# Optimization experiments

Hardware: AMD Instinct MI355X
Metric: run time of the kernel (lower is better)

## Reference

```python
import jax, jax.numpy as jnp
import numpy as np


def l2_normalize(x, eps=1e-12):
    return x / (jnp.linalg.norm(x, axis=-1, keepdims=True) + eps)


def setup_inputs() -> dict:
    key = jax.random.key(0)
    k1, k2, k3 = jax.random.split(key, 3)
    s, n, dim = 16384, 8192, 512
    img_emb = jax.random.normal(k1, (s, dim), dtype=jnp.float32)
    txt_emb = jax.random.normal(k2, (n, dim), dtype=jnp.float32)
    key_idx = jax.random.randint(k3, (s,), 0, n, dtype=jnp.int32)
    t_prime = jnp.asarray(np.log(10.0), dtype=jnp.float32)  # typical SigLIP init
    b = jnp.asarray(-10.0, dtype=jnp.float32)
    return {"img_emb": img_emb, "txt_emb": txt_emb, "key_idx": key_idx,
            "t_prime": t_prime, "b": b}


def reference(img_emb, txt_emb, key_idx, t_prime, b):
    s, dim = img_emb.shape
    n = txt_emb.shape[0]
    t = jnp.exp(t_prime)
    zimg = l2_normalize(img_emb)   # [s, d]
    ztxt = l2_normalize(txt_emb)   # [n, d]

    # [s, n] similarity logits
    all_pairs_logits = jnp.matmul(zimg, ztxt.T) * t + b
    true_positive_logits = all_pairs_logits[jnp.arange(s), key_idx]       # [s]
    potential_positive_losses = jax.nn.softplus(-true_positive_logits)    # [s]

    # grouped argmin over images sharing the same text key (vectorized segmented argmin)
    seg_min = jax.ops.segment_min(potential_positive_losses, key_idx, num_segments=n)  # [n], +inf if empty
    is_best = potential_positive_losses == seg_min[key_idx]                            # [s]
    cand_idx = jnp.where(is_best, jnp.arange(s), s)
    sel = jax.ops.segment_min(cand_idx, key_idx, num_segments=n)  # first minimal index per key; big if empty
    valid = sel < s                                                # [n]
    selected_img_global_indices = jnp.where(valid, sel, -1)
    zimg_selected = jnp.where(valid[:, None],
                              jnp.take(zimg, jnp.clip(sel, 0, s - 1), axis=0),
                              jnp.zeros((), dtype=zimg.dtype))     # [n, d]

    final_logits = jnp.matmul(zimg_selected, ztxt.T) * t + b       # [n, n]
    final_labels = 2.0 * jnp.eye(n, dtype=final_logits.dtype) - 1.0
    loss_terms = jax.nn.softplus(-(final_labels * final_logits))
    final_loss = jnp.sum(loss_terms) / n
    return final_loss, zimg_selected, ztxt, final_logits, selected_img_global_indices
```

## Files before the change

### kernel.cpp

```cpp
#include <hip/hip_runtime.h>
#include <hip/hip_bf16.h>

typedef short short8 __attribute__((ext_vector_type(8)));
typedef float f32x4 __attribute__((ext_vector_type(4)));

#define S_IMG 16384
#define N_TXT 8192
#define DIM   512

#if __has_builtin(__builtin_amdgcn_exp2f)
#define FAST_EXP2(x) __builtin_amdgcn_exp2f(x)
#else
#define FAST_EXP2(x) exp2f(x)
#endif
#if __has_builtin(__builtin_amdgcn_logf)
#define FAST_LOG2(x) __builtin_amdgcn_logf(x)
#else
#define FAST_LOG2(x) log2f(x)
#endif
#if __has_builtin(__builtin_amdgcn_sched_barrier)
#define SCHED_FENCE() __builtin_amdgcn_sched_barrier(0)
#else
#define SCHED_FENCE()
#endif

__device__ inline float softplus_f(float x) {
  float e = FAST_EXP2(-fabsf(x) * 1.44269504088896f);
  return fmaxf(x, 0.f) + 0.69314718055995f * FAST_LOG2(1.0f + e);
}

#define GLOAD16(g, l)                                                   \
  __builtin_amdgcn_global_load_lds(                                     \
      (const __attribute__((address_space(1))) void*)(g),               \
      (__attribute__((address_space(3))) void*)(l), 16, 0, 0)

__device__ inline unsigned short f2bf(float x) {
  unsigned u = __builtin_bit_cast(unsigned, x);
  unsigned r = (u + 0x7FFFu + ((u >> 16) & 1u)) >> 16;
  return (unsigned short)r;
}

__device__ inline double wave_reduce_add_d(double v) {
#pragma unroll
  for (int m = 32; m; m >>= 1) v += __shfl_xor(v, m, 64);
  return v;
}

__global__ __launch_bounds__(256) void k_norm_txt(const float* __restrict__ txt,
                                                  float* __restrict__ ztxt_f32,
                                                  unsigned short* __restrict__ Bbf) {
  int row  = blockIdx.x * 4 + (threadIdx.x >> 6);
  int lane = threadIdx.x & 63;
  const float* src = txt + (size_t)row * DIM;
  float4 v0 = reinterpret_cast<const float4*>(src)[lane];
  float4 v1 = reinterpret_cast<const float4*>(src)[lane + 64];
  double ss = (double)v0.x * v0.x + (double)v0.y * v0.y + (double)v0.z * v0.z + (double)v0.w * v0.w
            + (double)v1.x * v1.x + (double)v1.y * v1.y + (double)v1.z * v1.z + (double)v1.w * v1.w;
  ss = wave_reduce_add_d(ss);
  float sc = (float)(1.0 / (sqrt(ss) + 1e-12));
  float o[8] = {v0.x * sc, v0.y * sc, v0.z * sc, v0.w * sc,
                v1.x * sc, v1.y * sc, v1.z * sc, v1.w * sc};
  float* dst = ztxt_f32 + (size_t)row * DIM;
#pragma unroll
  for (int j = 0; j < 4; ++j) dst[4 * lane + j] = o[j];
#pragma unroll
  for (int j = 0; j < 4; ++j) dst[256 + 4 * lane + j] = o[4 + j];
  ushort4 p0 = make_ushort4(f2bf(o[0]), f2bf(o[1]), f2bf(o[2]), f2bf(o[3]));
  ushort4 p1 = make_ushort4(f2bf(o[4]), f2bf(o[5]), f2bf(o[6]), f2bf(o[7]));
  reinterpret_cast<ushort4*>(Bbf + (size_t)row * DIM)[lane]       = p0;
  reinterpret_cast<ushort4*>(Bbf + (size_t)row * DIM + 256)[lane] = p1;
}

__global__ __launch_bounds__(256) void k_img_loss(const float* __restrict__ img,
                                                  const float* __restrict__ ztxt_f32,
                                                  const int* __restrict__ key_idx,
                                                  const float* __restrict__ tp,
                                                  const float* __restrict__ bp,
                                                  unsigned long long* __restrict__ seg,
                                                  float* __restrict__ invnorm) {
  int row  = blockIdx.x * 4 + (threadIdx.x >> 6);
  int lane = threadIdx.x & 63;
  const float* src = img + (size_t)row * DIM;
  float4 a0 = reinterpret_cast<const float4*>(src)[lane];
  float4 a1 = reinterpret_cast<const float4*>(src)[lane + 64];
  int key = key_idx[row];
  const float* zt = ztxt_f32 + (size_t)key * DIM;
  float z0[4], z1[4];
#pragma unroll
  for (int j = 0; j < 4; ++j) z0[j] = zt[4 * lane + j];
#pragma unroll
  for (int j = 0; j < 4; ++j) z1[j] = zt[256 + 4 * lane + j];
  double ss = (double)a0.x * a0.x + (double)a0.y * a0.y + (double)a0.z * a0.z + (double)a0.w * a0.w
            + (double)a1.x * a1.x + (double)a1.y * a1.y + (double)a1.z * a1.z + (double)a1.w * a1.w;
  double dp = (double)a0.x * z0[0] + (double)a0.y * z0[1] + (double)a0.z * z0[2] + (double)a0.w * z0[3]
            + (double)a1.x * z1[0] + (double)a1.y * z1[1] + (double)a1.z * z1[2] + (double)a1.w * z1[3];
  ss = wave_reduce_add_d(ss);
  dp = wave_reduce_add_d(dp);
  if (lane == 0) {
    double inv = 1.0 / (sqrt(ss) + 1e-12);
    invnorm[row] = (float)inv;
    float t = expf(tp[0]);
    float logit = (float)(dp * inv) * t + bp[0];
    float loss = log1pf(expf(-logit));
    unsigned long long pk =
        ((unsigned long long)__builtin_bit_cast(unsigned, loss) << 32) | (unsigned)row;
    atomicMin(seg + key, pk);
  }
}

__global__ __launch_bounds__(256) void k_select(const float* __restrict__ img,
                                                const unsigned long long* __restrict__ seg,
                                                const float* __restrict__ invnorm,
                                                float* __restrict__ zsel_f32,
                                                float* __restrict__ idx_out,
                                                unsigned short* __restrict__ Abf) {
  int k    = blockIdx.x * 4 + (threadIdx.x >> 6);
  int lane = threadIdx.x & 63;
  unsigned long long pk = seg[k];
  float* dst = zsel_f32 + (size_t)k * DIM;
  float o[8];
  if (pk == 0xFFFFFFFFFFFFFFFFull) {
#pragma unroll
    for (int j = 0; j < 8; ++j) o[j] = 0.0f;
    if (lane == 0) idx_out[k] = -1.0f;
  } else {
    int sel = (int)(pk & 0xFFFFFFFFull);
    float invf = invnorm[sel];
    const float* src = img + (size_t)sel * DIM;
    float4 v0 = reinterpret_cast<const float4*>(src)[lane];
    float4 v1 = reinterpret_cast<const float4*>(src)[lane + 64];
    o[0] = v0.x * invf; o[1] = v0.y * invf; o[2] = v0.z * invf; o[3] = v0.w * invf;
    o[4] = v1.x * invf; o[5] = v1.y * invf; o[6] = v1.z * invf; o[7] = v1.w * invf;
    if (lane == 0) idx_out[k] = (float)sel;
  }
#pragma unroll
  for (int j = 0; j < 4; ++j) dst[4 * lane + j] = o[j];
#pragma unroll
  for (int j = 0; j < 4; ++j) dst[256 + 4 * lane + j] = o[4 + j];
  ushort4 p0 = make_ushort4(f2bf(o[0]), f2bf(o[1]), f2bf(o[2]), f2bf(o[3]));
  ushort4 p1 = make_ushort4(f2bf(o[4]), f2bf(o[5]), f2bf(o[6]), f2bf(o[7]));
  reinterpret_cast<ushort4*>(Abf + (size_t)k * DIM)[lane]       = p0;
  reinterpret_cast<ushort4*>(Abf + (size_t)k * DIM + 256)[lane] = p1;
}

#define BM 256
#define BN 256
#define BK 64
#define NT (DIM / BK)

__global__ __launch_bounds__(512, 2) void k_gemm(const unsigned short* __restrict__ A,
                                                 const unsigned short* __restrict__ B,
                                                 float* __restrict__ Cout,
                                                 const float* __restrict__ tp,
                                                 const float* __restrict__ bp,
                                                 float* __restrict__ part) {
  __shared__ __align__(16) unsigned short lds[2][4][128 * 64];
  int tid = threadIdx.x, lane = tid & 63, w = tid >> 6;
  int wm = w >> 2, wn = w & 3;

  int bid = blockIdx.x;
  int xcd = bid & 7, rr = bid >> 3;
  int bm = ((xcd << 2) + (rr & 3)) * BM;
  int bn = (rr >> 2) * BN;

  f32x4 acc[8][4] = {};
  int fr   = lane & 15;
  int ks0  = lane >> 4;
  int kso0 = ((ks0)     ^ (fr & 7)) * 8;
  int kso1 = ((ks0 + 4) ^ (fr & 7)) * 8;
  int brow = (wn & 1) * 64;

  int srow8 = lane >> 3;
  int scol  = ((lane & 7) ^ (srow8 & 7)) * 8;
  const unsigned short* gAh0 = A + (size_t)(bm + w * 16 + srow8) * DIM + scol;
  const unsigned short* gAh1 = gAh0 + (size_t)128 * DIM;
  const unsigned short* gBh0 = B + (size_t)(bn + w * 16 + srow8) * DIM + scol;
  const unsigned short* gBh1 = gBh0 + (size_t)128 * DIM;

#define STAGEH(buf, prt, g, kk)                                  \
  do {                                                           \
    GLOAD16((g) + (kk),           &lds[buf][prt][w * 1024]);     \
    GLOAD16((g) + (kk) + 8 * DIM, &lds[buf][prt][w * 1024 + 512]); \
  } while (0)

#define READQ(mh, nh)                                                              \
  _Pragma("unroll") for (int mm = 0; mm < 4; ++mm) {                               \
    afr[mm][0] = *reinterpret_cast<const short8*>(&LA[((mh * 4 + mm) * 16 + fr) * 64 + kso0]); \
    afr[mm][1] = *reinterpret_cast<const short8*>(&LA[((mh * 4 + mm) * 16 + fr) * 64 + kso1]); \
  }                                                                                \
  _Pragma("unroll") for (int nn = 0; nn < 2; ++nn) {                               \
    bfr[nn][0] = *reinterpret_cast<const short8*>(&LB[(brow + (nh * 2 + nn) * 16 + fr) * 64 + kso0]); \
    bfr[nn][1] = *reinterpret_cast<const short8*>(&LB[(brow + (nh * 2 + nn) * 16 + fr) * 64 + kso1]); \
  }

#define MFMAQ(mh, nh)                                                              \
  __builtin_amdgcn_s_setprio(1);                                                   \
  _Pragma("unroll") for (int mm = 0; mm < 4; ++mm)                                 \
    _Pragma("unroll") for (int nn = 0; nn < 2; ++nn) {                             \
      acc[mh * 4 + mm][nh * 2 + nn] = __builtin_amdgcn_mfma_f32_16x16x32_bf16(     \
          bfr[nn][0], afr[mm][0], acc[mh * 4 + mm][nh * 2 + nn], 0, 0, 0);         \
      acc[mh * 4 + mm][nh * 2 + nn] = __builtin_amdgcn_mfma_f32_16x16x32_bf16(     \
          bfr[nn][1], afr[mm][1], acc[mh * 4 + mm][nh * 2 + nn], 0, 0, 0);         \
    }                                                                              \
  __builtin_amdgcn_s_setprio(0);

  STAGEH(0, 0, gAh0, 0);
  STAGEH(0, 1, gAh1, 0);
  STAGEH(0, 2, gBh0, 0);
  STAGEH(0, 3, gBh1, 0);

  for (int t = 0; t < NT; ++t) {
    int buf = t & 1, nb = buf ^ 1;
    const unsigned short* LA = lds[buf][wm];
    const unsigned short* LB = lds[buf][2 + (wn >> 1)];
    int kk = (t + 1) * BK;
    if (t + 1 < NT) {
      STAGEH(nb, 0, gAh0, kk);
      asm volatile("s_waitcnt vmcnt(2)" ::: "memory");
    } else {
      asm volatile("s_waitcnt vmcnt(0)" ::: "memory");
    }
    __builtin_amdgcn_s_barrier();
    SCHED_FENCE();
    {
      short8 afr[4][2], bfr[2][2];
      READQ(0, 0)
      MFMAQ(0, 0)
    }
    __builtin_amdgcn_s_barrier();
    {
      short8 afr[4][2], bfr[2][2];
      READQ(0, 1)
      if (t + 1 < NT) STAGEH(nb, 1, gAh1, kk);
      __builtin_amdgcn_s_barrier();
      SCHED_FENCE();
      MFMAQ(0, 1)
    }
    __builtin_amdgcn_s_barrier();
    {
      short8 afr[4][2], bfr[2][2];
      READQ(1, 0)
      if (t + 1 < NT) STAGEH(nb, 2, gBh0, kk);
      __builtin_amdgcn_s_barrier();
      SCHED_FENCE();
      MFMAQ(1, 0)
    }
    __builtin_amdgcn_s_barrier();
    {
      short8 afr[4][2], bfr[2][2];
      READQ(1, 1)
      if (t + 1 < NT) STAGEH(nb, 3, gBh1, kk);
      __builtin_amdgcn_s_barrier();
      SCHED_FENCE();
      MFMAQ(1, 1)
    }
    __builtin_amdgcn_s_barrier();
  }

  float tt = expf(tp[0]), bb = bp[0];
  const float L2E = 1.44269504088896f;
  float local = 0.f;
  int orow = lane & 15;
  int oc4  = (lane >> 4) * 4;
  float* clds = reinterpret_cast<float*>(&lds[0][0][0]) + 1;
  int lr_r = tid >> 3, m8 = tid & 7;
#pragma unroll
  for (int p = 0; p < 4; ++p) {
    __syncthreads();
    if (wm == (p >> 1)) {
      int mbase = (p & 1) * 4;
#pragma unroll
      for (int mm = 0; mm < 4; ++mm) {
        int m = mbase + mm;
        int rowbase = bm + wm * 128 + m * 16;
        int lr = mm * 16 + orow;
#pragma unroll
        for (int n = 0; n < 4; ++n) {
          int colbase = bn + wn * 64 + n * 16;
          int lc = wn * 64 + n * 16 + oc4;
          float ov[4];
          if (rowbase == colbase) {
#pragma unroll
            for (int r2 = 0; r2 < 4; ++r2) {
              float logit = acc[m][n][r2] * tt + bb;
              ov[r2] = logit;
              float x = (orow == oc4 + r2) ? -logit : logit;
              local += softplus_f(x);
            }
          } else {
#pragma unroll
            for (int r2 = 0; r2 < 4; ++r2) {
              float logit = acc[m][n][r2] * tt + bb;
              ov[r2] = logit;
              float u = FAST_EXP2(logit * L2E);
              local += fmaf(-0.5f * u, u, u);
            }
          }
#pragma unroll
          for (int r2 = 0; r2 < 4; ++r2) clds[lr * 260 + lc + r2] = ov[r2];
        }
      }
    }
    __syncthreads();
    {
      float* gp = Cout + (size_t)(bm + p * 64 + lr_r) * N_TXT + bn;
      const float* lp = &clds[lr_r * 260];
#pragma unroll
      for (int K = 0; K < 7; ++K) {
        int c = 31 + 32 * K + 4 * m8;
        *reinterpret_cast<f32x4*>(gp + c) = *reinterpret_cast<const f32x4*>(lp + c);
      }
      if (m8 < 7) {
        int c = 3 + 4 * m8;
        *reinterpret_cast<f32x4*>(gp + c) = *reinterpret_cast<const f32x4*>(lp + c);
      }
      if (m8 < 3) gp[m8] = lp[m8];
      else if (m8 == 3) gp[255] = lp[255];
    }
  }
#pragma unroll
  for (int m = 32; m; m >>= 1) local += __shfl_xor(local, m, 64);
  __shared__ float wsum[8];
  if (lane == 0) wsum[w] = local;
  __syncthreads();
  if (tid == 0) {
    float sum = 0.f;
#pragma unroll
    for (int i = 0; i < 8; ++i) sum += wsum[i];
    part[bid] = sum;
  }
}

#define NPART 1024
__global__ __launch_bounds__(256) void k_final(const float* __restrict__ part,
                                               float* __restrict__ out0) {
  double s = 0.0;
  for (int i = threadIdx.x; i < NPART; i += 256) s += (double)part[i];
  s = wave_reduce_add_d(s);
  __shared__ double ws[4];
  if ((threadIdx.x & 63) == 0) ws[threadIdx.x >> 6] = s;
  __syncthreads();
  if (threadIdx.x == 0)
    out0[0] = (float)((ws[0] + ws[1] + ws[2] + ws[3]) / (double)N_TXT);
}

extern "C" void kernel_launch(void* const* d_in, const int* in_sizes, int n_in,
                              void* d_out, int out_size, void* d_ws, size_t ws_size,
                              hipStream_t stream) {
  const float* img = (const float*)d_in[0];
  const float* txt = (const float*)d_in[1];
  const int* key   = (const int*)d_in[2];
  const float* tp  = (const float*)d_in[3];
  const float* bp  = (const float*)d_in[4];

  float* out        = (float*)d_out;
  float* out_loss   = out;
  float* out_zsel   = out + 1;
  float* out_ztxt   = out_zsel + (size_t)N_TXT * DIM;
  float* out_logits = out_ztxt + (size_t)N_TXT * DIM;
  float* out_idx    = out_logits + (size_t)N_TXT * N_TXT;

  char* w = (char*)d_ws;
  unsigned long long* seg = (unsigned long long*)w;
  float* invnorm   = (float*)(w + 65536);
  float* part      = (float*)(w + 131072);
  unsigned short* Abf = (unsigned short*)(w + 131072 + 16384);
  unsigned short* Bbf = Abf + (size_t)N_TXT * DIM;
  size_t need = 131072 + 16384 + 2ull * N_TXT * DIM * sizeof(unsigned short);
  if (ws_size < need) return;

  (void)hipMemsetAsync(seg, 0xFF, (size_t)N_TXT * sizeof(unsigned long long), stream);

  k_norm_txt<<<N_TXT / 4, 256, 0, stream>>>(txt, out_ztxt, Bbf);
  k_img_loss<<<S_IMG / 4, 256, 0, stream>>>(img, out_ztxt, key, tp, bp, seg, invnorm);
  k_select<<<N_TXT / 4, 256, 0, stream>>>(img, seg, invnorm, out_zsel, out_idx, Abf);
  k_gemm<<<N_TXT / BM * (N_TXT / BN), 512, 0, stream>>>(Abf, Bbf, out_logits, tp, bp, part);
  k_final<<<1, 256, 0, stream>>>(part, out_loss);
}
```

Baseline: 163.5 us.

## Issue all next-tile loads up front and cut per-tile barriers to two

The K-loop used to split each tile into four quarter phases, each with its own LDS fragment reads and barrier, staggering the global-to-LDS stage of the next tile across them. It now issues all four stage loads for the next buffer at the start of the tile and waits with a larger vmcnt. B fragments are loaded once into registers for the whole tile and reused for both A halves, which removes repeated LDS reads of B and most intra-tile barriers. The cost is higher register pressure from holding four B fragment pairs, and the loads are no longer interleaved with compute, so memory and MFMA overlap depends on the hardware scheduler.

```diff
diff --git a/kernel.cpp b/kernel.cpp
--- a/kernel.cpp
+++ b/kernel.cpp
@@ -183,27 +183,6 @@
     GLOAD16((g) + (kk) + 8 * DIM, &lds[buf][prt][w * 1024 + 512]); \
   } while (0)
 
-#define READQ(mh, nh)                                                              \
-  _Pragma("unroll") for (int mm = 0; mm < 4; ++mm) {                               \
-    afr[mm][0] = *reinterpret_cast<const short8*>(&LA[((mh * 4 + mm) * 16 + fr) * 64 + kso0]); \
-    afr[mm][1] = *reinterpret_cast<const short8*>(&LA[((mh * 4 + mm) * 16 + fr) * 64 + kso1]); \
-  }                                                                                \
-  _Pragma("unroll") for (int nn = 0; nn < 2; ++nn) {                               \
-    bfr[nn][0] = *reinterpret_cast<const short8*>(&LB[(brow + (nh * 2 + nn) * 16 + fr) * 64 + kso0]); \
-    bfr[nn][1] = *reinterpret_cast<const short8*>(&LB[(brow + (nh * 2 + nn) * 16 + fr) * 64 + kso1]); \
-  }
-
-#define MFMAQ(mh, nh)                                                              \
-  __builtin_amdgcn_s_setprio(1);                                                   \
-  _Pragma("unroll") for (int mm = 0; mm < 4; ++mm)                                 \
-    _Pragma("unroll") for (int nn = 0; nn < 2; ++nn) {                             \
-      acc[mh * 4 + mm][nh * 2 + nn] = __builtin_amdgcn_mfma_f32_16x16x32_bf16(     \
-          bfr[nn][0], afr[mm][0], acc[mh * 4 + mm][nh * 2 + nn], 0, 0, 0);         \
-      acc[mh * 4 + mm][nh * 2 + nn] = __builtin_amdgcn_mfma_f32_16x16x32_bf16(     \
-          bfr[nn][1], afr[mm][1], acc[mh * 4 + mm][nh * 2 + nn], 0, 0, 0);         \
-    }                                                                              \
-  __builtin_amdgcn_s_setprio(0);
-
   STAGEH(0, 0, gAh0, 0);
   STAGEH(0, 1, gAh1, 0);
   STAGEH(0, 2, gBh0, 0);
@@ -216,43 +195,54 @@
     int kk = (t + 1) * BK;
     if (t + 1 < NT) {
       STAGEH(nb, 0, gAh0, kk);
-      asm volatile("s_waitcnt vmcnt(2)" ::: "memory");
+      STAGEH(nb, 1, gAh1, kk);
+      STAGEH(nb, 2, gBh0, kk);
+      STAGEH(nb, 3, gBh1, kk);
+      asm volatile("s_waitcnt vmcnt(8)" ::: "memory");
     } else {
       asm volatile("s_waitcnt vmcnt(0)" ::: "memory");
     }
     __builtin_amdgcn_s_barrier();
     SCHED_FENCE();
+    short8 bfr[4][2];
+#pragma unroll
+    for (int n = 0; n < 4; ++n) {
+      bfr[n][0] = *reinterpret_cast<const short8*>(&LB[(brow + n * 16 + fr) * 64 + kso0]);
+      bfr[n][1] = *reinterpret_cast<const short8*>(&LB[(brow + n * 16 + fr) * 64 + kso1]);
+    }
     {
-      short8 afr[4][2], bfr[2][2];
-      READQ(0, 0)
-      MFMAQ(0, 0)
-    }
-    __builtin_amdgcn_s_barrier();
+      short8 afr[4][2];
+#pragma unroll
+      for (int mm = 0; mm < 4; ++mm) {
+        afr[mm][0] = *reinterpret_cast<const short8*>(&LA[(mm * 16 + fr) * 64 + kso0]);
+        afr[mm][1] = *reinterpret_cast<const short8*>(&LA[(mm * 16 + fr) * 64 + kso1]);
+      }
+      __builtin_amdgcn_s_setprio(1);
+#pragma unroll
+      for (int mm = 0; mm < 4; ++mm)
+#pragma unroll
+        for (int n = 0; n < 4; ++n) {
+          acc[mm][n] = __builtin_amdgcn_mfma_f32_16x16x32_bf16(bfr[n][0], afr[mm][0], acc[mm][n], 0, 0, 0);
+          acc[mm][n] = __builtin_amdgcn_mfma_f32_16x16x32_bf16(bfr[n][1], afr[mm][1], acc[mm][n], 0, 0, 0);
+        }
+      __builtin_amdgcn_s_setprio(0);
+    }
     {
-      short8 afr[4][2], bfr[2][2];
-      READQ(0, 1)
-      if (t + 1 < NT) STAGEH(nb, 1, gAh1, kk);
-      __builtin_amdgcn_s_barrier();
-      SCHED_FENCE();
-      MFMAQ(0, 1)
-    }
-    __builtin_amdgcn_s_barrier();
-    {
-      short8 afr[4][2], bfr[2][2];
-      READQ(1, 0)
-      if (t + 1 < NT) STAGEH(nb, 2, gBh0, kk);
-      __builtin_amdgcn_s_barrier();
-      SCHED_FENCE();
-      MFMAQ(1, 0)
-    }
-    __builtin_amdgcn_s_barrier();
-    {
-      short8 afr[4][2], bfr[2][2];
-      READQ(1, 1)
-      if (t + 1 < NT) STAGEH(nb, 3, gBh1, kk);
-      __builtin_amdgcn_s_barrier();
-      SCHED_FENCE();
-      MFMAQ(1, 1)
+      short8 afr[4][2];
+#pragma unroll
+      for (int mm = 0; mm < 4; ++mm) {
+        afr[mm][0] = *reinterpret_cast<const short8*>(&LA[((4 + mm) * 16 + fr) * 64 + kso0]);
+        afr[mm][1] = *reinterpret_cast<const short8*>(&LA[((4 + mm) * 16 + fr) * 64 + kso1]);
+      }
+      __builtin_amdgcn_s_setprio(1);
+#pragma unroll
+      for (int mm = 0; mm < 4; ++mm)
+#pragma unroll
+        for (int n = 0; n < 4; ++n) {
+          acc[4 + mm][n] = __builtin_amdgcn_mfma_f32_16x16x32_bf16(bfr[n][0], afr[mm][0], acc[4 + mm][n], 0, 0, 0);
+          acc[4 + mm][n] = __builtin_amdgcn_mfma_f32_16x16x32_bf16(bfr[n][1], afr[mm][1], acc[4 + mm][n], 0, 0, 0);
+        }
+      __builtin_amdgcn_s_setprio(0);
     }
     __builtin_amdgcn_s_barrier();
   }
@@ -273,11 +263,11 @@
       for (int mm = 0; mm < 4; ++mm) {
         int m = mbase + mm;
         int rowbase = bm + wm * 128 + m * 16;
-        int lr = mm * 16 + orow;
 #pragma unroll
         for (int n = 0; n < 4; ++n) {
           int colbase = bn + wn * 64 + n * 16;
           int lc = wn * 64 + n * 16 + oc4;
+          int lr = mm * 16 + orow;
           float ov[4];
           if (rowbase == colbase) {
 #pragma unroll
```

After: 158.5 us. -3.1%, faster.
